# Kernel optimization log

Measured on AMD Instinct MI355X. Metric: run time of the kernel, lower is better.

Reference implementation:

```python
import jax, jax.numpy as jnp
import numpy as np

H = 16
D_MODEL = 1024
D_K = D_MODEL // H
B, S = 4, 2048


def setup_inputs() -> dict:
    key = jax.random.key(0)
    ks = jax.random.split(key, 12)
    scale = 1.0 / np.sqrt(D_MODEL)
    inp = {
        "query": jax.random.normal(ks[0], (B, S, D_MODEL), jnp.float32),
        "key_in": jax.random.normal(ks[1], (B, S, D_MODEL), jnp.float32),
        "value": jax.random.normal(ks[2], (B, S, D_MODEL), jnp.float32),
        "mask": jax.random.randint(ks[3], (B, 1, S, S), 0, 2, jnp.int32),
    }
    # 4 Linear(d_model, d_model) layers: Wq, Wk, Wv, Wo (+ biases)
    names = ["q", "k", "v", "o"]
    for i, n in enumerate(names):
        inp[f"W{n}"] = jax.random.normal(ks[4 + i], (D_MODEL, D_MODEL), jnp.float32) * scale
        inp[f"b{n}"] = jax.random.normal(ks[8 + i], (D_MODEL,), jnp.float32) * scale
    return inp


def reference(query, key_in, value, mask, Wq, bq, Wk, bk, Wv, bv, Wo, bo):
    # Linear projections then split heads: [B,S,D] -> [B,H,S,Dk]
    def proj(x, W, b):
        y = jnp.einsum("bsd,ed->bse", x, W) + b  # torch Linear: x @ W.T + b
        return y.reshape(B, S, H, D_K).transpose(0, 2, 1, 3)

    q = proj(query, Wq, bq)
    k = proj(key_in, Wk, bk)
    v = proj(value, Wv, bv)

    scores = jnp.einsum("bhqd,bhkd->bhqk", q, k) / jnp.sqrt(jnp.float32(D_K))
    scores = jnp.where(mask == 0, jnp.float32(-1e9), scores)
    p_attn = jax.nn.softmax(scores, axis=-1)
    # dropout is identity in eval mode
    x = jnp.einsum("bhqk,bhkd->bhqd", p_attn, v)
    x = x.transpose(0, 2, 1, 3).reshape(B, S, D_MODEL)
    return jnp.einsum("bsd,ed->bse", x, Wo) + bo
```

## Files before the change

### kernel.cpp

```cpp
#include <hip/hip_runtime.h>
#include <hip/hip_bf16.h>

typedef __bf16 bf16_t;
typedef __attribute__((ext_vector_type(8))) __bf16 bf16x8;
typedef __attribute__((ext_vector_type(4))) __bf16 bf16x4;
typedef __attribute__((ext_vector_type(4))) float f32x4;

#define GAS __attribute__((address_space(1)))
#define LAS __attribute__((address_space(3)))

__device__ __forceinline__ void async_copy16(const bf16_t* g, bf16_t* l) {
    __builtin_amdgcn_global_load_lds((const GAS void*)g, (LAS void*)l, 16, 0, 0);
}

__global__ __launch_bounds__(256) void convert_kernel(
    const float* __restrict__ src, bf16_t* __restrict__ dst, int n)
{
    int i = (blockIdx.x * 256 + threadIdx.x) * 8;
    if (i >= n) return;
    f32x4 f0 = *(const f32x4*)(src + i);
    f32x4 f1 = *(const f32x4*)(src + i + 4);
    bf16x8 v;
#pragma unroll
    for (int j = 0; j < 4; j++) { v[j] = (bf16_t)f0[j]; v[4 + j] = (bf16_t)f1[j]; }
    *(bf16x8*)&dst[i] = v;
}

__global__ __launch_bounds__(256) void pack_mask_kernel(
    const int* __restrict__ mask, unsigned long long* __restrict__ out)
{
    int i = blockIdx.x * 256 + threadIdx.x;
    unsigned long long bits = __ballot(mask[i] != 0);
    if ((threadIdx.x & 63) == 0) out[i >> 6] = bits;
}

template<int MODE>
__global__ __launch_bounds__(256, 2) void gemm_nt(
    const bf16_t* __restrict__ A, const bf16_t* __restrict__ W,
    const float* __restrict__ bias, void* __restrict__ out_, float oscale)
{
    __shared__ __align__(16) bf16_t Als[128 * 32];
    __shared__ __align__(16) bf16_t Bls[128 * 32];

    const int tid  = threadIdx.x;
    const int wave = tid >> 6, lane = tid & 63;
    const int quad = lane >> 4, lq = lane & 15;
    const int wm = wave >> 1, wn = wave & 1;
    const int tm = blockIdx.x * 128, tn = blockIdx.y * 128;
    const int K = 1024;

    const bf16_t* gA0 = A + (size_t)(tm + wave * 32 + (lane >> 2)) * K + (lane & 3) * 8;
    const bf16_t* gA1 = gA0 + (size_t)16 * K;
    const bf16_t* gB0 = W + (size_t)(tn + wave * 32 + (lane >> 2)) * K + (lane & 3) * 8;
    const bf16_t* gB1 = gB0 + (size_t)16 * K;
    bf16_t* lA0 = &Als[(wave * 32) * 32];
    bf16_t* lA1 = &Als[(wave * 32 + 16) * 32];
    bf16_t* lB0 = &Bls[(wave * 32) * 32];
    bf16_t* lB1 = &Bls[(wave * 32 + 16) * 32];

    f32x4 acc[4][4] = {};

    for (int k0 = 0; k0 < K; k0 += 32) {
        __syncthreads();
        async_copy16(gA0, lA0);
        async_copy16(gA1, lA1);
        async_copy16(gB0, lB0);
        async_copy16(gB1, lB1);
        gA0 += 32; gA1 += 32; gB0 += 32; gB1 += 32;
        __syncthreads();

        bf16x8 af[4], bfr[4];
#pragma unroll
        for (int i = 0; i < 4; i++) {
            af[i]  = *(const bf16x8*)&Als[(wm * 64 + i * 16 + lq) * 32 + quad * 8];
            bfr[i] = *(const bf16x8*)&Bls[(wn * 64 + i * 16 + lq) * 32 + quad * 8];
        }
#pragma unroll
        for (int i = 0; i < 4; i++)
#pragma unroll
            for (int j = 0; j < 4; j++) {
                if (MODE == 2)
                    acc[i][j] = __builtin_amdgcn_mfma_f32_16x16x32_bf16(bfr[j], af[i], acc[i][j], 0, 0, 0);
                else
                    acc[i][j] = __builtin_amdgcn_mfma_f32_16x16x32_bf16(af[i], bfr[j], acc[i][j], 0, 0, 0);
            }
    }

    float* outf = (float*)out_;
    bf16_t* outb = (bf16_t*)out_;
#pragma unroll
    for (int i = 0; i < 4; i++)
#pragma unroll
        for (int j = 0; j < 4; j++)
#pragma unroll
            for (int r = 0; r < 4; r++) {
                float v = acc[i][j][r];
                if (MODE == 0) {
                    int row = tm + wm * 64 + i * 16 + quad * 4 + r;
                    int col = tn + wn * 64 + j * 16 + lq;
                    outf[(size_t)row * 1024 + col] = (v + bias[col]) * oscale;
                } else if (MODE == 1) {
                    int row = tm + wm * 64 + i * 16 + quad * 4 + r;
                    int col = tn + wn * 64 + j * 16 + lq;
                    v = (v + bias[col]) * oscale;
                    int b = row >> 11, s = row & 2047;
                    int h = col >> 6,  dk = col & 63;
                    outb[(((size_t)(b * 16 + h) * 2048 + s) << 6) + dk] = (bf16_t)v;
                } else {
                    int n = tn + wn * 64 + j * 16 + quad * 4 + r;
                    int m = tm + wm * 64 + i * 16 + lq;
                    v = (v + bias[n]) * oscale;
                    int b = m >> 11, s = m & 2047;
                    int h = n >> 6,  dk = n & 63;
                    outb[((size_t)((b * 16 + h) * 64 + dk) << 11) + s] = (bf16_t)v;
                }
            }
}

#define LDK 72
#define LDV 72
#define LDP 72

__global__ __launch_bounds__(256, 4) void attn_kernel(
    const bf16_t* __restrict__ Q, const bf16_t* __restrict__ Kh,
    const bf16_t* __restrict__ Vt, const unsigned int* __restrict__ mp,
    bf16_t* __restrict__ X)
{
    __shared__ __align__(16) bf16_t Kls[64 * LDK];
    __shared__ __align__(16) bf16_t Vls[64 * LDV];
    __shared__ __align__(16) bf16_t Pls[4][32 * LDP];

    const int tid  = threadIdx.x;
    const int wave = tid >> 6, lane = tid & 63;
    const int quad = lane >> 4, lq = lane & 15;
    const int bh = blockIdx.y;
    const int b  = bh >> 4, h = bh & 15;
    const int qwv = blockIdx.x * 128 + wave * 32;

    bf16x8 qf[2][2];
#pragma unroll
    for (int qs = 0; qs < 2; qs++) {
        const bf16_t* qptr = Q + ((size_t)bh * 2048 + qwv + qs * 16 + lq) * 64 + quad * 8;
        qf[qs][0] = *(const bf16x8*)qptr;
        qf[qs][1] = *(const bf16x8*)(qptr + 32);
    }

    f32x4 o[2][4] = {};
    f32x4 ls[2] = {};

    const int sr = tid >> 3, sc = tid & 7;
    const bf16_t* gK0 = Kh + ((size_t)bh * 2048 + sr) * 64 + sc * 8;
    const bf16_t* gK1 = gK0 + 32 * 64;
    const bf16_t* gV0 = Vt + ((size_t)bh * 64 + sr) * 2048 + sc * 8;
    const bf16_t* gV1 = gV0 + 32 * 2048;
    bf16_t* lK0 = &Kls[sr * LDK + sc * 8];
    bf16_t* lK1 = &Kls[(sr + 32) * LDK + sc * 8];
    bf16_t* lV0 = &Vls[sr * LDV + sc * 8];
    bf16_t* lV1 = &Vls[(sr + 32) * LDV + sc * 8];

    const unsigned int* mr0 = mp + ((size_t)(b << 11) + qwv + lq) * 64;

    bf16x8 ks0 = *(const bf16x8*)gK0, ks1 = *(const bf16x8*)gK1;
    bf16x8 vs0 = *(const bf16x8*)gV0, vs1 = *(const bf16x8*)gV1;

    for (int kt = 0; kt < 32; kt++) {
        __syncthreads();
        *(bf16x8*)lK0 = ks0; *(bf16x8*)lK1 = ks1;
        *(bf16x8*)lV0 = vs0; *(bf16x8*)lV1 = vs1;
        __syncthreads();
        if (kt < 31) {
            gK0 += 4096; gK1 += 4096; gV0 += 64; gV1 += 64;
            ks0 = *(const bf16x8*)gK0; ks1 = *(const bf16x8*)gK1;
            vs0 = *(const bf16x8*)gV0; vs1 = *(const bf16x8*)gV1;
        }
        unsigned int w[2][2];
        w[0][0] = mr0[2 * kt];        w[0][1] = mr0[2 * kt + 1];
        w[1][0] = mr0[2 * kt + 1024]; w[1][1] = mr0[2 * kt + 1025];

        bf16_t* pb = &Pls[wave][0];
#pragma unroll
        for (int nt = 0; nt < 4; nt++) {
            const bf16_t* krow = &Kls[(nt * 16 + lq) * LDK];
            bf16x8 kf0 = *(const bf16x8*)(krow + quad * 8);
            bf16x8 kf1 = *(const bf16x8*)(krow + 32 + quad * 8);
#pragma unroll
            for (int qs = 0; qs < 2; qs++) {
                f32x4 z = {};
                z = __builtin_amdgcn_mfma_f32_16x16x32_bf16(kf0, qf[qs][0], z, 0, 0, 0);
                z = __builtin_amdgcn_mfma_f32_16x16x32_bf16(kf1, qf[qs][1], z, 0, 0, 0);
                unsigned int wq = w[qs][nt >> 1] >> ((nt & 1) * 16 + quad * 4);
                bf16x4 pk;
#pragma unroll
                for (int r = 0; r < 4; r++) {
                    float sv = ((wq >> r) & 1) ? z[r] : -1e9f;
                    float p = __expf(sv);
                    ls[qs][r] += p;
                    pk[r] = (bf16_t)p;
                }
                *(bf16x4*)&pb[(qs * 16 + lq) * LDP + nt * 16 + quad * 4] = pk;
            }
        }

#pragma unroll
        for (int c = 0; c < 2; c++) {
            bf16x8 pf0 = *(const bf16x8*)&pb[lq * LDP + c * 32 + quad * 8];
            bf16x8 pf1 = *(const bf16x8*)&pb[(16 + lq) * LDP + c * 32 + quad * 8];
#pragma unroll
            for (int dt = 0; dt < 4; dt++) {
                bf16x8 vf = *(const bf16x8*)&Vls[(dt * 16 + lq) * LDV + c * 32 + quad * 8];
                o[0][dt] = __builtin_amdgcn_mfma_f32_16x16x32_bf16(pf0, vf, o[0][dt], 0, 0, 0);
                o[1][dt] = __builtin_amdgcn_mfma_f32_16x16x32_bf16(pf1, vf, o[1][dt], 0, 0, 0);
            }
        }
    }

#pragma unroll
    for (int qs = 0; qs < 2; qs++) {
        float l = (ls[qs][0] + ls[qs][1]) + (ls[qs][2] + ls[qs][3]);
        l += __shfl_xor(l, 16);
        l += __shfl_xor(l, 32);
        float rl[4];
#pragma unroll
        for (int r = 0; r < 4; r++) {
            float lv = __shfl(l, quad * 4 + r);
            rl[r] = (lv > 0.f) ? 1.0f / lv : 0.f;
        }
#pragma unroll
        for (int dt = 0; dt < 4; dt++)
#pragma unroll
            for (int r = 0; r < 4; r++) {
                int qrow = qwv + qs * 16 + quad * 4 + r;
                X[((size_t)(b * 2048) + qrow) * 1024 + h * 64 + dt * 16 + lq] =
                    (bf16_t)(o[qs][dt][r] * rl[r]);
            }
    }
}

extern "C" void kernel_launch(void* const* d_in, const int* in_sizes, int n_in,
                              void* d_out, int out_size, void* d_ws, size_t ws_size,
                              hipStream_t stream)
{
    const float* query  = (const float*)d_in[0];
    const float* key_in = (const float*)d_in[1];
    const float* value  = (const float*)d_in[2];
    const int*   mask   = (const int*)d_in[3];

    char* ws = (char*)d_ws;
    const size_t SZ  = (size_t)8192 * 1024 * 2;
    const size_t MPK = (size_t)2 * 1024 * 1024;
    const size_t WSZ = (size_t)1024 * 1024 * 2;
    bf16_t* C   = (bf16_t*)(ws);
    bf16_t* Qb  = (bf16_t*)(ws + SZ);
    bf16_t* Kb  = (bf16_t*)(ws + 2 * SZ);
    bf16_t* Vtb = (bf16_t*)(ws + 3 * SZ);
    unsigned long long* mpack = (unsigned long long*)(ws + 4 * SZ);
    bf16_t* Wc[4];
    for (int i = 0; i < 4; i++)
        Wc[i] = (bf16_t*)(ws + 4 * SZ + MPK + i * WSZ);

    const size_t NEED = 4 * SZ + MPK + 4 * WSZ;
    if (ws_size < NEED) return;

    const int NACT = 8192 * 1024;
    for (int i = 0; i < 4; i++)
        convert_kernel<<<512, 256, 0, stream>>>((const float*)d_in[4 + 2 * i],
                                                Wc[i], 1024 * 1024);
    pack_mask_kernel<<<65536, 256, 0, stream>>>(mask, mpack);

    dim3 gg(64, 8);
    convert_kernel<<<4096, 256, 0, stream>>>(query, C, NACT);
    gemm_nt<1><<<gg, 256, 0, stream>>>(C, Wc[0], (const float*)d_in[5], Qb, 0.125f);
    convert_kernel<<<4096, 256, 0, stream>>>(key_in, C, NACT);
    gemm_nt<1><<<gg, 256, 0, stream>>>(C, Wc[1], (const float*)d_in[7], Kb, 1.0f);
    convert_kernel<<<4096, 256, 0, stream>>>(value, C, NACT);
    gemm_nt<2><<<gg, 256, 0, stream>>>(C, Wc[2], (const float*)d_in[9], Vtb, 1.0f);

    attn_kernel<<<dim3(16, 64), 256, 0, stream>>>(Qb, Kb, Vtb,
                                                  (const unsigned int*)mpack, C);
    gemm_nt<0><<<gg, 256, 0, stream>>>(C, Wc[3], (const float*)d_in[11], d_out, 1.0f);
}
```

Baseline: 443.0 us.

## Fuse activation conversion into QKV GEMM, batch launches, read V directly

The separate fp32-to-bf16 activation conversion kernels are dropped. The QKV GEMM now loads fp32 activations, converts them in registers and stores them to LDS, and all three projections run in a single 3D-grid launch. The four weight conversions are merged into one launch. The attention kernel no longer stages V in LDS and reads V fragments straight from global memory, with occupancy hint changed from 4 to 2. This removes the extra activation round trips and several launches, at the cost of synchronous fp32 A loads in the GEMM and uncoalesced-ish global V reads in attention.

```diff
diff --git a/kernel.cpp b/kernel.cpp
--- a/kernel.cpp
+++ b/kernel.cpp
@@ -13,11 +13,17 @@
     __builtin_amdgcn_global_load_lds((const GAS void*)g, (LAS void*)l, 16, 0, 0);
 }
 
-__global__ __launch_bounds__(256) void convert_kernel(
-    const float* __restrict__ src, bf16_t* __restrict__ dst, int n)
-{
+struct WConvArgs {
+    const float *s0, *s1, *s2, *s3;
+    bf16_t *d0, *d1, *d2, *d3;
+};
+
+__global__ __launch_bounds__(256) void wconv_kernel(WConvArgs a)
+{
+    const int seg = blockIdx.y;
+    const float* src = seg == 0 ? a.s0 : seg == 1 ? a.s1 : seg == 2 ? a.s2 : a.s3;
+    bf16_t*     dst = seg == 0 ? a.d0 : seg == 1 ? a.d1 : seg == 2 ? a.d2 : a.d3;
     int i = (blockIdx.x * 256 + threadIdx.x) * 8;
-    if (i >= n) return;
     f32x4 f0 = *(const f32x4*)(src + i);
     f32x4 f1 = *(const f32x4*)(src + i + 4);
     bf16x8 v;
@@ -34,13 +40,25 @@
     if ((threadIdx.x & 63) == 0) out[i >> 6] = bits;
 }
 
-template<int MODE>
-__global__ __launch_bounds__(256, 2) void gemm_nt(
-    const bf16_t* __restrict__ A, const bf16_t* __restrict__ W,
-    const float* __restrict__ bias, void* __restrict__ out_, float oscale)
+struct QKVArgs {
+    const float *A0, *A1, *A2;
+    const bf16_t *W0, *W1, *W2;
+    const float *b0, *b1, *b2;
+    bf16_t *o0, *o1, *o2;
+};
+
+__global__ __launch_bounds__(256, 2) void qkv_gemm(QKVArgs g)
 {
     __shared__ __align__(16) bf16_t Als[128 * 32];
     __shared__ __align__(16) bf16_t Bls[128 * 32];
+
+    const int z = blockIdx.z;
+    const float*  A    = z == 0 ? g.A0 : z == 1 ? g.A1 : g.A2;
+    const bf16_t* W    = z == 0 ? g.W0 : z == 1 ? g.W1 : g.W2;
+    const float*  bias = z == 0 ? g.b0 : z == 1 ? g.b1 : g.b2;
+    bf16_t*       outb = z == 0 ? g.o0 : z == 1 ? g.o1 : g.o2;
+    const float oscale = (z == 0) ? 0.125f : 1.0f;
+    const bool  vmode  = (z == 2);
 
     const int tid  = threadIdx.x;
     const int wave = tid >> 6, lane = tid & 63;
@@ -49,12 +67,12 @@
     const int tm = blockIdx.x * 128, tn = blockIdx.y * 128;
     const int K = 1024;
 
-    const bf16_t* gA0 = A + (size_t)(tm + wave * 32 + (lane >> 2)) * K + (lane & 3) * 8;
-    const bf16_t* gA1 = gA0 + (size_t)16 * K;
+    const float*  gA0 = A + (size_t)(tm + wave * 32 + (lane >> 2)) * K + (lane & 3) * 8;
+    const float*  gA1 = gA0 + (size_t)16 * K;
     const bf16_t* gB0 = W + (size_t)(tn + wave * 32 + (lane >> 2)) * K + (lane & 3) * 8;
     const bf16_t* gB1 = gB0 + (size_t)16 * K;
-    bf16_t* lA0 = &Als[(wave * 32) * 32];
-    bf16_t* lA1 = &Als[(wave * 32 + 16) * 32];
+    bf16_t* lA0 = &Als[(wave * 32 + (lane >> 2)) * 32 + (lane & 3) * 8];
+    bf16_t* lA1 = lA0 + 16 * 32;
     bf16_t* lB0 = &Bls[(wave * 32) * 32];
     bf16_t* lB1 = &Bls[(wave * 32 + 16) * 32];
 
@@ -62,11 +80,19 @@
 
     for (int k0 = 0; k0 < K; k0 += 32) {
         __syncthreads();
-        async_copy16(gA0, lA0);
-        async_copy16(gA1, lA1);
         async_copy16(gB0, lB0);
         async_copy16(gB1, lB1);
+        f32x4 a00 = *(const f32x4*)gA0, a01 = *(const f32x4*)(gA0 + 4);
+        f32x4 a10 = *(const f32x4*)gA1, a11 = *(const f32x4*)(gA1 + 4);
         gA0 += 32; gA1 += 32; gB0 += 32; gB1 += 32;
+        bf16x8 av0, av1;
+#pragma unroll
+        for (int j = 0; j < 4; j++) {
+            av0[j] = (bf16_t)a00[j]; av0[4 + j] = (bf16_t)a01[j];
+            av1[j] = (bf16_t)a10[j]; av1[4 + j] = (bf16_t)a11[j];
+        }
+        *(bf16x8*)lA0 = av0;
+        *(bf16x8*)lA1 = av1;
         __syncthreads();
 
         bf16x8 af[4], bfr[4];
@@ -75,19 +101,21 @@
             af[i]  = *(const bf16x8*)&Als[(wm * 64 + i * 16 + lq) * 32 + quad * 8];
             bfr[i] = *(const bf16x8*)&Bls[(wn * 64 + i * 16 + lq) * 32 + quad * 8];
         }
-#pragma unroll
-        for (int i = 0; i < 4; i++)
-#pragma unroll
-            for (int j = 0; j < 4; j++) {
-                if (MODE == 2)
+        if (vmode) {
+#pragma unroll
+            for (int i = 0; i < 4; i++)
+#pragma unroll
+                for (int j = 0; j < 4; j++)
                     acc[i][j] = __builtin_amdgcn_mfma_f32_16x16x32_bf16(bfr[j], af[i], acc[i][j], 0, 0, 0);
-                else
+        } else {
+#pragma unroll
+            for (int i = 0; i < 4; i++)
+#pragma unroll
+                for (int j = 0; j < 4; j++)
                     acc[i][j] = __builtin_amdgcn_mfma_f32_16x16x32_bf16(af[i], bfr[j], acc[i][j], 0, 0, 0);
-            }
-    }
-
-    float* outf = (float*)out_;
-    bf16_t* outb = (bf16_t*)out_;
+        }
+    }
+
 #pragma unroll
     for (int i = 0; i < 4; i++)
 #pragma unroll
@@ -95,11 +123,7 @@
 #pragma unroll
             for (int r = 0; r < 4; r++) {
                 float v = acc[i][j][r];
-                if (MODE == 0) {
-                    int row = tm + wm * 64 + i * 16 + quad * 4 + r;
-                    int col = tn + wn * 64 + j * 16 + lq;
-                    outf[(size_t)row * 1024 + col] = (v + bias[col]) * oscale;
-                } else if (MODE == 1) {
+                if (!vmode) {
                     int row = tm + wm * 64 + i * 16 + quad * 4 + r;
                     int col = tn + wn * 64 + j * 16 + lq;
                     v = (v + bias[col]) * oscale;
@@ -109,7 +133,7 @@
                 } else {
                     int n = tn + wn * 64 + j * 16 + quad * 4 + r;
                     int m = tm + wm * 64 + i * 16 + lq;
-                    v = (v + bias[n]) * oscale;
+                    v = v + bias[n];
                     int b = m >> 11, s = m & 2047;
                     int h = n >> 6,  dk = n & 63;
                     outb[((size_t)((b * 16 + h) * 64 + dk) << 11) + s] = (bf16_t)v;
@@ -117,17 +141,74 @@
             }
 }
 
+__global__ __launch_bounds__(256, 2) void gemm_o(
+    const bf16_t* __restrict__ A, const bf16_t* __restrict__ W,
+    const float* __restrict__ bias, float* __restrict__ outf)
+{
+    __shared__ __align__(16) bf16_t Als[128 * 32];
+    __shared__ __align__(16) bf16_t Bls[128 * 32];
+
+    const int tid  = threadIdx.x;
+    const int wave = tid >> 6, lane = tid & 63;
+    const int quad = lane >> 4, lq = lane & 15;
+    const int wm = wave >> 1, wn = wave & 1;
+    const int tm = blockIdx.x * 128, tn = blockIdx.y * 128;
+    const int K = 1024;
+
+    const bf16_t* gA0 = A + (size_t)(tm + wave * 32 + (lane >> 2)) * K + (lane & 3) * 8;
+    const bf16_t* gA1 = gA0 + (size_t)16 * K;
+    const bf16_t* gB0 = W + (size_t)(tn + wave * 32 + (lane >> 2)) * K + (lane & 3) * 8;
+    const bf16_t* gB1 = gB0 + (size_t)16 * K;
+    bf16_t* lA0 = &Als[(wave * 32) * 32];
+    bf16_t* lA1 = &Als[(wave * 32 + 16) * 32];
+    bf16_t* lB0 = &Bls[(wave * 32) * 32];
+    bf16_t* lB1 = &Bls[(wave * 32 + 16) * 32];
+
+    f32x4 acc[4][4] = {};
+
+    for (int k0 = 0; k0 < K; k0 += 32) {
+        __syncthreads();
+        async_copy16(gA0, lA0);
+        async_copy16(gA1, lA1);
+        async_copy16(gB0, lB0);
+        async_copy16(gB1, lB1);
+        gA0 += 32; gA1 += 32; gB0 += 32; gB1 += 32;
+        __syncthreads();
+
+        bf16x8 af[4], bfr[4];
+#pragma unroll
+        for (int i = 0; i < 4; i++) {
+            af[i]  = *(const bf16x8*)&Als[(wm * 64 + i * 16 + lq) * 32 + quad * 8];
+            bfr[i] = *(const bf16x8*)&Bls[(wn * 64 + i * 16 + lq) * 32 + quad * 8];
+        }
+#pragma unroll
+        for (int i = 0; i < 4; i++)
+#pragma unroll
+            for (int j = 0; j < 4; j++)
+                acc[i][j] = __builtin_amdgcn_mfma_f32_16x16x32_bf16(af[i], bfr[j], acc[i][j], 0, 0, 0);
+    }
+
+#pragma unroll
+    for (int i = 0; i < 4; i++)
+#pragma unroll
+        for (int j = 0; j < 4; j++)
+#pragma unroll
+            for (int r = 0; r < 4; r++) {
+                int row = tm + wm * 64 + i * 16 + quad * 4 + r;
+                int col = tn + wn * 64 + j * 16 + lq;
+                outf[(size_t)row * 1024 + col] = acc[i][j][r] + bias[col];
+            }
+}
+
 #define LDK 72
-#define LDV 72
 #define LDP 72
 
-__global__ __launch_bounds__(256, 4) void attn_kernel(
+__global__ __launch_bounds__(256, 2) void attn_kernel(
     const bf16_t* __restrict__ Q, const bf16_t* __restrict__ Kh,
     const bf16_t* __restrict__ Vt, const unsigned int* __restrict__ mp,
     bf16_t* __restrict__ X)
 {
     __shared__ __align__(16) bf16_t Kls[64 * LDK];
-    __shared__ __align__(16) bf16_t Vls[64 * LDV];
     __shared__ __align__(16) bf16_t Pls[4][32 * LDP];
 
     const int tid  = threadIdx.x;
@@ -151,27 +232,22 @@
     const int sr = tid >> 3, sc = tid & 7;
     const bf16_t* gK0 = Kh + ((size_t)bh * 2048 + sr) * 64 + sc * 8;
     const bf16_t* gK1 = gK0 + 32 * 64;
-    const bf16_t* gV0 = Vt + ((size_t)bh * 64 + sr) * 2048 + sc * 8;
-    const bf16_t* gV1 = gV0 + 32 * 2048;
     bf16_t* lK0 = &Kls[sr * LDK + sc * 8];
     bf16_t* lK1 = &Kls[(sr + 32) * LDK + sc * 8];
-    bf16_t* lV0 = &Vls[sr * LDV + sc * 8];
-    bf16_t* lV1 = &Vls[(sr + 32) * LDV + sc * 8];
+
+    const bf16_t* vrow = Vt + ((size_t)bh * 64 + lq) * 2048 + quad * 8;
 
     const unsigned int* mr0 = mp + ((size_t)(b << 11) + qwv + lq) * 64;
 
     bf16x8 ks0 = *(const bf16x8*)gK0, ks1 = *(const bf16x8*)gK1;
-    bf16x8 vs0 = *(const bf16x8*)gV0, vs1 = *(const bf16x8*)gV1;
 
     for (int kt = 0; kt < 32; kt++) {
         __syncthreads();
         *(bf16x8*)lK0 = ks0; *(bf16x8*)lK1 = ks1;
-        *(bf16x8*)lV0 = vs0; *(bf16x8*)lV1 = vs1;
         __syncthreads();
         if (kt < 31) {
-            gK0 += 4096; gK1 += 4096; gV0 += 64; gV1 += 64;
+            gK0 += 4096; gK1 += 4096;
             ks0 = *(const bf16x8*)gK0; ks1 = *(const bf16x8*)gK1;
-            vs0 = *(const bf16x8*)gV0; vs1 = *(const bf16x8*)gV1;
         }
         unsigned int w[2][2];
         w[0][0] = mr0[2 * kt];        w[0][1] = mr0[2 * kt + 1];
@@ -205,9 +281,10 @@
         for (int c = 0; c < 2; c++) {
             bf16x8 pf0 = *(const bf16x8*)&pb[lq * LDP + c * 32 + quad * 8];
             bf16x8 pf1 = *(const bf16x8*)&pb[(16 + lq) * LDP + c * 32 + quad * 8];
+            const size_t voff = (size_t)(kt * 64 + c * 32);
 #pragma unroll
             for (int dt = 0; dt < 4; dt++) {
-                bf16x8 vf = *(const bf16x8*)&Vls[(dt * 16 + lq) * LDV + c * 32 + quad * 8];
+                bf16x8 vf = *(const bf16x8*)(vrow + (size_t)dt * 16 * 2048 + voff);
                 o[0][dt] = __builtin_amdgcn_mfma_f32_16x16x32_bf16(pf0, vf, o[0][dt], 0, 0, 0);
                 o[1][dt] = __builtin_amdgcn_mfma_f32_16x16x32_bf16(pf1, vf, o[1][dt], 0, 0, 0);
             }
@@ -249,7 +326,7 @@
     const size_t SZ  = (size_t)8192 * 1024 * 2;
     const size_t MPK = (size_t)2 * 1024 * 1024;
     const size_t WSZ = (size_t)1024 * 1024 * 2;
-    bf16_t* C   = (bf16_t*)(ws);
+    bf16_t* X   = (bf16_t*)(ws);
     bf16_t* Qb  = (bf16_t*)(ws + SZ);
     bf16_t* Kb  = (bf16_t*)(ws + 2 * SZ);
     bf16_t* Vtb = (bf16_t*)(ws + 3 * SZ);
@@ -261,21 +338,20 @@
     const size_t NEED = 4 * SZ + MPK + 4 * WSZ;
     if (ws_size < NEED) return;
 
-    const int NACT = 8192 * 1024;
-    for (int i = 0; i < 4; i++)
-        convert_kernel<<<512, 256, 0, stream>>>((const float*)d_in[4 + 2 * i],
-                                                Wc[i], 1024 * 1024);
+    WConvArgs wa = { (const float*)d_in[4], (const float*)d_in[6],
+                     (const float*)d_in[8], (const float*)d_in[10],
+                     Wc[0], Wc[1], Wc[2], Wc[3] };
+    wconv_kernel<<<dim3(512, 4), 256, 0, stream>>>(wa);
     pack_mask_kernel<<<65536, 256, 0, stream>>>(mask, mpack);
 
-    dim3 gg(64, 8);
-    convert_kernel<<<4096, 256, 0, stream>>>(query, C, NACT);
-    gemm_nt<1><<<gg, 256, 0, stream>>>(C, Wc[0], (const float*)d_in[5], Qb, 0.125f);
-    convert_kernel<<<4096, 256, 0, stream>>>(key_in, C, NACT);
-    gemm_nt<1><<<gg, 256, 0, stream>>>(C, Wc[1], (const float*)d_in[7], Kb, 1.0f);
-    convert_kernel<<<4096, 256, 0, stream>>>(value, C, NACT);
-    gemm_nt<2><<<gg, 256, 0, stream>>>(C, Wc[2], (const float*)d_in[9], Vtb, 1.0f);
+    QKVArgs qa = { query, key_in, value,
+                   Wc[0], Wc[1], Wc[2],
+                   (const float*)d_in[5], (const float*)d_in[7], (const float*)d_in[9],
+                   Qb, Kb, Vtb };
+    qkv_gemm<<<dim3(64, 8, 3), 256, 0, stream>>>(qa);
 
     attn_kernel<<<dim3(16, 64), 256, 0, stream>>>(Qb, Kb, Vtb,
-                                                  (const unsigned int*)mpack, C);
-    gemm_nt<0><<<gg, 256, 0, stream>>>(C, Wc[3], (const float*)d_in[11], d_out, 1.0f);
-}
+                                                  (const unsigned int*)mpack, X);
+    gemm_o<<<dim3(64, 8), 256, 0, stream>>>(X, Wc[3], (const float*)d_in[11],
+                                            (float*)d_out);
+}
```

After: 542.5 us. 1.22x slower.

## Swizzle attention K/V LDS layout, merge weight conversions, relax attn occupancy

Applied to the files above, without the earlier changes.

Applies an XOR swizzle to the K and V shared-memory tiles in the attention kernel, so the 16-byte fragment reads by lanes 8-15 use a different column than lanes 0-7. The aim is to cut LDS bank conflicts in the QK and PV MFMA loops. It also merges the four weight fp32-to-bf16 conversion launches into one 2D-grid launch to save launch overhead. Attention launch bounds drop from 4 to 2 blocks per CU, which gives the compiler more registers but may lower occupancy. An empty leftover loop was added and has no effect.

```diff
diff --git a/kernel.cpp b/kernel.cpp
--- a/kernel.cpp
+++ b/kernel.cpp
@@ -18,6 +18,25 @@
 {
     int i = (blockIdx.x * 256 + threadIdx.x) * 8;
     if (i >= n) return;
+    f32x4 f0 = *(const f32x4*)(src + i);
+    f32x4 f1 = *(const f32x4*)(src + i + 4);
+    bf16x8 v;
+#pragma unroll
+    for (int j = 0; j < 4; j++) { v[j] = (bf16_t)f0[j]; v[4 + j] = (bf16_t)f1[j]; }
+    *(bf16x8*)&dst[i] = v;
+}
+
+struct WConvArgs {
+    const float *s0, *s1, *s2, *s3;
+    bf16_t *d0, *d1, *d2, *d3;
+};
+
+__global__ __launch_bounds__(256) void wconv_kernel(WConvArgs a)
+{
+    const int seg = blockIdx.y;
+    const float* src = seg == 0 ? a.s0 : seg == 1 ? a.s1 : seg == 2 ? a.s2 : a.s3;
+    bf16_t*     dst = seg == 0 ? a.d0 : seg == 1 ? a.d1 : seg == 2 ? a.d2 : a.d3;
+    int i = (blockIdx.x * 256 + threadIdx.x) * 8;
     f32x4 f0 = *(const f32x4*)(src + i);
     f32x4 f1 = *(const f32x4*)(src + i + 4);
     bf16x8 v;
@@ -121,7 +140,7 @@
 #define LDV 72
 #define LDP 72
 
-__global__ __launch_bounds__(256, 4) void attn_kernel(
+__global__ __launch_bounds__(256, 2) void attn_kernel(
     const bf16_t* __restrict__ Q, const bf16_t* __restrict__ Kh,
     const bf16_t* __restrict__ Vt, const unsigned int* __restrict__ mp,
     bf16_t* __restrict__ X)
@@ -133,6 +152,7 @@
     const int tid  = threadIdx.x;
     const int wave = tid >> 6, lane = tid & 63;
     const int quad = lane >> 4, lq = lane & 15;
+    const int xr8  = lq & 8;
     const int bh = blockIdx.y;
     const int b  = bh >> 4, h = bh & 15;
     const int qwv = blockIdx.x * 128 + wave * 32;
@@ -153,10 +173,11 @@
     const bf16_t* gK1 = gK0 + 32 * 64;
     const bf16_t* gV0 = Vt + ((size_t)bh * 64 + sr) * 2048 + sc * 8;
     const bf16_t* gV1 = gV0 + 32 * 2048;
-    bf16_t* lK0 = &Kls[sr * LDK + sc * 8];
-    bf16_t* lK1 = &Kls[(sr + 32) * LDK + sc * 8];
-    bf16_t* lV0 = &Vls[sr * LDV + sc * 8];
-    bf16_t* lV1 = &Vls[(sr + 32) * LDV + sc * 8];
+    const int swc = (sc * 8) ^ (sr & 8);
+    bf16_t* lK0 = &Kls[sr * LDK + swc];
+    bf16_t* lK1 = &Kls[(sr + 32) * LDK + swc];
+    bf16_t* lV0 = &Vls[sr * LDV + swc];
+    bf16_t* lV1 = &Vls[(sr + 32) * LDV + swc];
 
     const unsigned int* mr0 = mp + ((size_t)(b << 11) + qwv + lq) * 64;
 
@@ -179,10 +200,13 @@
 
         bf16_t* pb = &Pls[wave][0];
 #pragma unroll
+        for (int nt = 0; nt < 2; nt++) {
+        }
+#pragma unroll
         for (int nt = 0; nt < 4; nt++) {
             const bf16_t* krow = &Kls[(nt * 16 + lq) * LDK];
-            bf16x8 kf0 = *(const bf16x8*)(krow + quad * 8);
-            bf16x8 kf1 = *(const bf16x8*)(krow + 32 + quad * 8);
+            bf16x8 kf0 = *(const bf16x8*)(krow + ((quad * 8) ^ xr8));
+            bf16x8 kf1 = *(const bf16x8*)(krow + 32 + ((quad * 8) ^ xr8));
 #pragma unroll
             for (int qs = 0; qs < 2; qs++) {
                 f32x4 z = {};
@@ -207,7 +231,8 @@
             bf16x8 pf1 = *(const bf16x8*)&pb[(16 + lq) * LDP + c * 32 + quad * 8];
 #pragma unroll
             for (int dt = 0; dt < 4; dt++) {
-                bf16x8 vf = *(const bf16x8*)&Vls[(dt * 16 + lq) * LDV + c * 32 + quad * 8];
+                bf16x8 vf = *(const bf16x8*)&Vls[(dt * 16 + lq) * LDV +
+                                                 (c * 32 + ((quad * 8) ^ xr8))];
                 o[0][dt] = __builtin_amdgcn_mfma_f32_16x16x32_bf16(pf0, vf, o[0][dt], 0, 0, 0);
                 o[1][dt] = __builtin_amdgcn_mfma_f32_16x16x32_bf16(pf1, vf, o[1][dt], 0, 0, 0);
             }
@@ -262,9 +287,10 @@
     if (ws_size < NEED) return;
 
     const int NACT = 8192 * 1024;
-    for (int i = 0; i < 4; i++)
-        convert_kernel<<<512, 256, 0, stream>>>((const float*)d_in[4 + 2 * i],
-                                                Wc[i], 1024 * 1024);
+    WConvArgs wa = { (const float*)d_in[4], (const float*)d_in[6],
+                     (const float*)d_in[8], (const float*)d_in[10],
+                     Wc[0], Wc[1], Wc[2], Wc[3] };
+    wconv_kernel<<<dim3(512, 4), 256, 0, stream>>>(wa);
     pack_mask_kernel<<<65536, 256, 0, stream>>>(mask, mpack);
 
     dim3 gg(64, 8);
```

Measured after the change: 437.5 us. No clear change (-1.2%).
